# Performance work log

Hardware: AMD Instinct MI355X
Metric: run time of the kernel (lower is better)

Reference implementation:

```python
import jax, jax.numpy as jnp
import numpy as np

N, T, D = 2048, 32, 256
NE = T + 2                       # num_embeddings = 32 + 3 - 1
GK_MUL, GK_NUM = 2.0, 3
HEADS = (4, 1)

def _bn(x, g, b):
    # BatchNorm1d (training-mode batch stats, biased variance, eps=1e-5)
    m = x.mean(0)
    v = jnp.mean((x - m) ** 2, 0)
    return (x - m) * jax.lax.rsqrt(v + 1e-5) * g + b

def _gk(x):
    # multi-bandwidth Gaussian kernel over pairwise squared L2 distances
    sq = jnp.sum(x * x, -1)
    l2 = jnp.maximum(sq[:, None] + sq[None, :] - 2.0 * (x @ x.T), 0.0)
    n = x.shape[0]
    bw = jnp.sum(l2) / (n * n - n) / (GK_MUL ** (GK_NUM // 2))
    out = jnp.zeros_like(l2)
    for i in range(GK_NUM):
        out = out + jnp.exp(-l2 / (bw * (GK_MUL ** i)))
    return out

def _mlp3(x, w, b):
    h = jax.nn.relu(x @ w[0] + b[0])
    h = jax.nn.relu(h @ w[1] + b[1])
    return h @ w[2] + b[2]

def _ln(x, g, b):
    m = x.mean(-1, keepdims=True)
    v = jnp.mean((x - m) ** 2, -1, keepdims=True)
    return (x - m) * jax.lax.rsqrt(v + 1e-5) * g + b

def _posenc(t, d):
    pos = jnp.arange(t, dtype=jnp.float32)[:, None]
    div = jnp.exp(jnp.arange(0, d, 2, dtype=jnp.float32) * (-np.log(10000.0) / d))
    ang = pos * div
    return jnp.stack([jnp.sin(ang), jnp.cos(ang)], -1).reshape(t, d)

def _tlayer(x, mask, w, b, w1, b1, w2, b2, g, be, h):
    n, l, d = x.shape
    dh = d // h
    def split(t):
        return t.reshape(n, l, h, dh).transpose(0, 2, 1, 3)
    q = split(x @ w[0] + b[0])
    k = split(x @ w[1] + b[1])
    v = split(x @ w[2] + b[2])
    s = jnp.einsum('bhld,bhmd->bhlm', q, k) / np.sqrt(dh)
    s = jnp.where(mask[:, None, :, :], s, -1e9)
    o = jnp.einsum('bhlm,bhmd->bhld', jax.nn.softmax(s, -1), v)
    o = o.transpose(0, 2, 1, 3).reshape(n, l, d)
    x = _ln(x + o @ w[3] + b[3], g[0], be[0])
    f = jax.nn.relu(x @ w1 + b1) @ w2 + b2
    return _ln(x + f, g[1], be[1])

def _forward(emb0, emb1, emb2, simi_w, simi_b, bn_g, bn_b, simi_eps, dissim,
             gcn_w, gcn_b, adapt_w, adapt_b, type_emb, attn_w, attn_b,
             ffn_w1, ffn_b1, ffn_w2, ffn_b2, ln_g, ln_b,
             out_w1, out_b1, out_w2, out_b2, msk0, msk1, msk2):
    n = emb0.shape[0]
    embs = [emb0[:, 0, :], emb1, emb2]
    msks = [msk0[:, :1], msk1, msk2]               # [n,1] bool each
    mstk = jnp.stack(msks)                         # [3,n,1]
    mask_mats = mstk & jnp.swapaxes(mstk, 1, 2)    # [3,n,n]
    sim_sum = jnp.zeros((n, n), emb0.dtype)
    lstab = jnp.zeros((), emb0.dtype)
    for m in range(3):
        e = embs[m]
        p = _mlp3(e, simi_w[m], simi_b[m])
        wgk = _gk(_bn(jax.nn.relu(p), bn_g, bn_b))
        gk = _gk(_bn(e, bn_g, bn_b))
        eps = jax.nn.sigmoid(simi_eps[m])
        sim_sum = sim_sum + ((1.0 - eps) * wgk + eps) * gk * mask_mats[m]
        lstab = lstab + jnp.abs(jnp.linalg.norm(p) - jnp.linalg.norm(e))
    agg = sim_sum / mask_mats.sum(0).astype(emb0.dtype)
    agg = agg * (agg > jax.nn.sigmoid(dissim[0]))
    imputed = []
    for m in range(3):  # all modals are missing-capable
        h = jax.nn.relu(agg @ (embs[m] @ gcn_w[m, 0]) + gcn_b[m, 0])
        h = jax.nn.relu(agg @ (h @ gcn_w[m, 1]) + gcn_b[m, 1])
        s = jax.nn.sigmoid(embs[m] @ adapt_w[m].T + adapt_b[m])
        o = jax.nn.sigmoid(h @ adapt_w[m].T + adapt_b[m])  # adapt_self reused, bug kept from source
        s = s / (s + o)
        imp = s * embs[m] + (1.0 - s) * h
        mk = msks[m].astype(emb0.dtype)
        imputed.append(imp * mk + (1.0 - mk) * h)
    e0 = emb0.at[:, 0, :].set(imputed[0]) + type_emb[0]
    e0 = e0 + _posenc(emb0.shape[1], emb0.shape[2])
    e1 = imputed[1][:, None, :] + type_emb[1]
    e2 = imputed[2][:, None, :] + type_emb[2]
    z = jnp.concatenate([e0, e1, e2], 1)            # [n, NE, D]
    tok = jnp.concatenate([msk0, msk1, msk2], 1)    # [n, NE]
    amask = tok[:, :, None] & tok[:, None, :]       # [n, NE, NE]
    for li in range(2):
        z = jax.nn.relu(_tlayer(z, amask, attn_w[li], attn_b[li],
                                ffn_w1[li], ffn_b1[li], ffn_w2[li], ffn_b2[li],
                                ln_g[li], ln_b[li], HEADS[li]))
    comb = z.reshape(n, -1)
    y = jax.nn.relu(comb @ out_w1 + out_b1)
    y = (y @ out_w2 + out_b2).squeeze(-1)
    return y, lstab

def setup_inputs():
    key = jax.random.key(0)
    it = iter(jax.random.split(key, 32))
    def nrm(shape, s):
        return jax.random.normal(next(it), shape, jnp.float32) * s
    return {
        'emb0': nrm((N, T, D), 1.0),
        'emb1': nrm((N, D), 1.0),
        'emb2': nrm((N, D), 1.0),
        'msk0': jax.random.randint(next(it), (N, T), 0, 2).astype(bool),
        'msk1': jnp.ones((N, 1), bool),
        'msk2': jax.random.randint(next(it), (N, 1), 0, 2).astype(bool),
        'simi_w': nrm((3, 3, D, D), 0.06), 'simi_b': jnp.zeros((3, 3, D)),
        'bn_g': jnp.ones((D,)), 'bn_b': jnp.zeros((D,)),
        'simi_eps': jnp.ones((4,)), 'dissim': jnp.full((1,), 2.0),
        'gcn_w': nrm((3, 2, D, D), 0.06), 'gcn_b': jnp.zeros((3, 2, D)),
        'adapt_w': nrm((3, 1, D), 0.06), 'adapt_b': jnp.zeros((3, 1)),
        'type_emb': nrm((3, D), 0.02),
        'attn_w': nrm((2, 4, D, D), 0.06), 'attn_b': jnp.zeros((2, 4, D)),
        'ffn_w1': nrm((2, D, 4 * D), 0.06), 'ffn_b1': jnp.zeros((2, 4 * D)),
        'ffn_w2': nrm((2, 4 * D, D), 0.06), 'ffn_b2': jnp.zeros((2, D)),
        'ln_g': jnp.ones((2, 2, D)), 'ln_b': jnp.zeros((2, 2, D)),
        'out_w1': nrm((NE * D, 2 * D), 0.02), 'out_b1': jnp.zeros((2 * D,)),
        'out_w2': nrm((2 * D, 1), 0.02), 'out_b2': jnp.zeros((1,)),
    }

def reference(emb0, emb1, emb2, msk0, msk1, msk2, simi_w, simi_b, bn_g, bn_b,
              simi_eps, dissim, gcn_w, gcn_b, adapt_w, adapt_b, type_emb,
              attn_w, attn_b, ffn_w1, ffn_b1, ffn_w2, ffn_b2, ln_g, ln_b,
              out_w1, out_b1, out_w2, out_b2):
    return _forward(emb0, emb1, emb2, simi_w, simi_b, bn_g, bn_b, simi_eps,
                    dissim, gcn_w, gcn_b, adapt_w, adapt_b, type_emb, attn_w,
                    attn_b, ffn_w1, ffn_b1, ffn_w2, ffn_b2, ln_g, ln_b,
                    out_w1, out_b1, out_w2, out_b2, msk0, msk1, msk2)
```

## Files before the change

kernel.cpp:

```cpp
#include <hip/hip_runtime.h>
#include <hip/hip_bf16.h>


#define NN 2048
#define DD 256
#define LTOK 34

typedef __attribute__((ext_vector_type(8))) short bf16x8;
typedef __attribute__((ext_vector_type(4))) float f32x4;

__device__ __forceinline__ float bf2f(__hip_bfloat16 x) { return __bfloat162float(x); }
__device__ __forceinline__ __hip_bfloat16 f2bf(float x) { return __float2bfloat16(x); }
__device__ __forceinline__ float us2f(ushort u) {
    unsigned x = (unsigned)u << 16;
    float f;
    __builtin_memcpy(&f, &x, 4);
    return f;
}
__device__ __forceinline__ ushort f2us(float x) {
    __hip_bfloat16 h = f2bf(x);
    ushort u;
    __builtin_memcpy(&u, &h, 2);
    return u;
}

__device__ __forceinline__ float block_reduce_sum256(float v, float* red) {
    for (int o = 32; o > 0; o >>= 1) v += __shfl_down(v, o, 64);
    int tid = threadIdx.x;
    if ((tid & 63) == 0) red[tid >> 6] = v;
    __syncthreads();
    float s = red[0] + red[1] + red[2] + red[3];
    __syncthreads();
    return s;
}

__device__ __forceinline__ int xcd_remap(int lin, int nwg) {
    int q = nwg >> 3, r = nwg & 7;
    int xcd = lin & 7, pos = lin >> 3;
    return (xcd < r ? xcd * (q + 1) : r * (q + 1) + (xcd - r) * q) + pos;
}

__device__ __forceinline__ void stage_tile(const ushort* __restrict__ src,
                                           ushort* lds, int grow0, size_t ldk,
                                           int k0, int wv, int l) {
#pragma unroll
    for (int c = 0; c < 4; ++c) {
        int rowbase = wv * 32 + c * 8;
        int row = rowbase + (l >> 3);
        int sx = ((l & 7) ^ (row & 7)) * 8;
        __builtin_amdgcn_global_load_lds(
            (const __attribute__((address_space(1))) void*)(src + (size_t)(grow0 + row) * ldk + k0 + sx),
            (__attribute__((address_space(3))) void*)(lds + rowbase * 64), 16, 0, 0);
    }
}

__device__ __forceinline__ void stage_tile64(const ushort* __restrict__ src,
                                             ushort* lds, int grow0, size_t ldk,
                                             int k0, int wv, int l) {
#pragma unroll
    for (int c = 0; c < 2; ++c) {
        int rowbase = wv * 16 + c * 8;
        int row = rowbase + (l >> 3);
        int sx = ((l & 7) ^ (row & 7)) * 8;
        __builtin_amdgcn_global_load_lds(
            (const __attribute__((address_space(1))) void*)(src + (size_t)(grow0 + row) * ldk + k0 + sx),
            (__attribute__((address_space(3))) void*)(lds + rowbase * 64), 16, 0, 0);
    }
}

#define MFMA_STEP(ACC)                                                          \
    {                                                                           \
        bf16x8 av[4], bv[4];                                                    \
        _Pragma("unroll") for (int f = 0; f < 4; ++f) {                         \
            int ra = wr * 64 + f * 16 + lr;                                     \
            av[f] = *(const bf16x8*)(As + ra * 64 + (((kk * 4 + l16) ^ (ra & 7)) * 8)); \
            int rb = wc * 64 + f * 16 + lr;                                     \
            bv[f] = *(const bf16x8*)(Bs + rb * 64 + (((kk * 4 + l16) ^ (rb & 7)) * 8)); \
        }                                                                       \
        _Pragma("unroll") for (int mf = 0; mf < 4; ++mf)                        \
            _Pragma("unroll") for (int nf = 0; nf < 4; ++nf)                    \
                ACC[mf][nf] = __builtin_amdgcn_mfma_f32_16x16x32_bf16(          \
                    av[mf], bv[nf], ACC[mf][nf], 0, 0, 0);                      \
    }

#define MFMA_STEP_T(ACC)                                                        \
    {                                                                           \
        bf16x8 av[2], bv[4];                                                    \
        _Pragma("unroll") for (int f = 0; f < 2; ++f) {                         \
            int ra = wr * 32 + f * 16 + lr;                                     \
            av[f] = *(const bf16x8*)(As + ra * 64 + (((kk * 4 + l16) ^ (ra & 7)) * 8)); \
        }                                                                       \
        _Pragma("unroll") for (int f = 0; f < 4; ++f) {                         \
            int rb = wc * 64 + f * 16 + lr;                                     \
            bv[f] = *(const bf16x8*)(Bs + rb * 64 + (((kk * 4 + l16) ^ (rb & 7)) * 8)); \
        }                                                                       \
        _Pragma("unroll") for (int mf = 0; mf < 2; ++mf)                        \
            _Pragma("unroll") for (int nf = 0; nf < 4; ++nf)                    \
                ACC[mf][nf] = __builtin_amdgcn_mfma_f32_16x16x32_bf16(          \
                    av[mf], bv[nf], ACC[mf][nf], 0, 0, 0);                      \
    }

template <int OUTM, bool BIAS, bool RELU>
__global__ __launch_bounds__(256) void gemm_mfma(
    const ushort* __restrict__ A, const ushort* __restrict__ Bt,
    const float* __restrict__ bias, void* __restrict__ Cout,
    int M, int N, int K)
{
    __shared__ __align__(16) ushort As[128 * 64];
    __shared__ __align__(16) ushort Bs[128 * 64];
    const int gx = gridDim.x;
    int lin = xcd_remap(blockIdx.y * gx + blockIdx.x, gx * gridDim.y);
    const int bm = (lin / gx) * 128, bn = (lin % gx) * 128;
    const int tid = threadIdx.x;
    const int l = tid & 63, wv = tid >> 6;
    const int wr = wv >> 1, wc = wv & 1;
    const int l16 = l >> 4, lr = l & 15;
    const int kpz = K / gridDim.z;
    const int kbeg = blockIdx.z * kpz, kend = kbeg + kpz;
    f32x4 zero = {0.f, 0.f, 0.f, 0.f};
    f32x4 acc[4][4];
#pragma unroll
    for (int i = 0; i < 4; ++i)
#pragma unroll
        for (int j = 0; j < 4; ++j) acc[i][j] = zero;

    for (int k0 = kbeg; k0 < kend; k0 += 64) {
        stage_tile(A, As, bm, K, k0, wv, l);
        stage_tile(Bt, Bs, bn, K, k0, wv, l);
        __syncthreads();
#pragma unroll
        for (int kk = 0; kk < 2; ++kk) MFMA_STEP(acc)
        __syncthreads();
    }
    float* Cf = (float*)Cout + (size_t)blockIdx.z * M * N;
    __hip_bfloat16* Cb = (__hip_bfloat16*)Cout + (size_t)blockIdx.z * M * N;
#pragma unroll
    for (int mf = 0; mf < 4; ++mf) {
#pragma unroll
        for (int nf = 0; nf < 4; ++nf) {
            int col = bn + wc * 64 + nf * 16 + lr;
            float bb = BIAS ? bias[col] : 0.f;
#pragma unroll
            for (int r = 0; r < 4; ++r) {
                int row = bm + wr * 64 + mf * 16 + l16 * 4 + r;
                float v = acc[mf][nf][r] + bb;
                if (OUTM == 3)
                    v += bf2f(((const __hip_bfloat16*)Cout)[(size_t)row * N + col]);
                if (RELU) v = fmaxf(v, 0.f);
                if (OUTM == 0)
                    Cf[(size_t)row * N + col] = v;
                else if (OUTM == 5)
                    Cb[(size_t)row * N + col] = f2bf(v);
                else
                    ((__hip_bfloat16*)Cout)[(size_t)row * N + col] = f2bf(v);
            }
        }
    }
}

template <int OUTM, bool BIAS, bool RELU>
__global__ __launch_bounds__(256) void gemm_thin(
    const ushort* __restrict__ A, const ushort* __restrict__ Bt,
    const float* __restrict__ bias, void* __restrict__ Cout,
    int M, int N, int K)
{
    __shared__ __align__(16) ushort As[64 * 64];
    __shared__ __align__(16) ushort Bs[128 * 64];
    const int gx = gridDim.x;
    int lin = xcd_remap(blockIdx.y * gx + blockIdx.x, gx * gridDim.y);
    const int bm = (lin / gx) * 64, bn = (lin % gx) * 128;
    const int tid = threadIdx.x;
    const int l = tid & 63, wv = tid >> 6;
    const int wr = wv >> 1, wc = wv & 1;
    const int l16 = l >> 4, lr = l & 15;
    f32x4 zero = {0.f, 0.f, 0.f, 0.f};
    f32x4 acc[2][4];
#pragma unroll
    for (int i = 0; i < 2; ++i)
#pragma unroll
        for (int j = 0; j < 4; ++j) acc[i][j] = zero;

    for (int k0 = 0; k0 < K; k0 += 64) {
        stage_tile64(A, As, bm, K, k0, wv, l);
        stage_tile(Bt, Bs, bn, K, k0, wv, l);
        __syncthreads();
#pragma unroll
        for (int kk = 0; kk < 2; ++kk) MFMA_STEP_T(acc)
        __syncthreads();
    }
#pragma unroll
    for (int mf = 0; mf < 2; ++mf) {
#pragma unroll
        for (int nf = 0; nf < 4; ++nf) {
            int col = bn + wc * 64 + nf * 16 + lr;
            float bb = BIAS ? bias[col] : 0.f;
#pragma unroll
            for (int r = 0; r < 4; ++r) {
                int row = bm + wr * 32 + mf * 16 + l16 * 4 + r;
                float v = acc[mf][nf][r] + bb;
                if (OUTM == 3)
                    v += bf2f(((const __hip_bfloat16*)Cout)[(size_t)row * N + col]);
                if (RELU) v = fmaxf(v, 0.f);
                ((__hip_bfloat16*)Cout)[(size_t)row * N + col] = f2bf(v);
            }
        }
    }
}

template <int OUTM, bool RELU, bool BIAS, bool PSUM>
__global__ __launch_bounds__(256) void gemm_batch_t(
    const ushort* __restrict__ A, int lda, size_t aoffZ,
    const ushort* __restrict__ Bt, size_t boffZ,
    const float* __restrict__ bias, int biasoffZ,
    void* __restrict__ Cout, int ldc, size_t coffZ,
    float* __restrict__ psum, int M, int N, int K)
{
    __shared__ __align__(16) ushort As[64 * 64];
    __shared__ __align__(16) ushort Bs[128 * 64];
    __shared__ float red[8];
    const int gx = gridDim.x;
    const int lin0 = blockIdx.y * gx + blockIdx.x;
    int lin = xcd_remap(lin0, gx * gridDim.y);
    const int bm = (lin / gx) * 64, bn = (lin % gx) * 128;
    const int z = blockIdx.z;
    A += (size_t)z * aoffZ;
    Bt += (size_t)z * boffZ;
    if (BIAS) bias += (size_t)z * biasoffZ;
    const int tid = threadIdx.x;
    const int l = tid & 63, wv = tid >> 6;
    const int wr = wv >> 1, wc = wv & 1;
    const int l16 = l >> 4, lr = l & 15;
    f32x4 zero = {0.f, 0.f, 0.f, 0.f};
    f32x4 acc[2][4];
#pragma unroll
    for (int i = 0; i < 2; ++i)
#pragma unroll
        for (int j = 0; j < 4; ++j) acc[i][j] = zero;

    for (int k0 = 0; k0 < K; k0 += 64) {
        stage_tile64(A, As, bm, lda, k0, wv, l);
        stage_tile(Bt, Bs, bn, K, k0, wv, l);
        __syncthreads();
#pragma unroll
        for (int kk = 0; kk < 2; ++kk) MFMA_STEP_T(acc)
        __syncthreads();
    }
    float lsq = 0.f;
#pragma unroll
    for (int mf = 0; mf < 2; ++mf) {
#pragma unroll
        for (int nf = 0; nf < 4; ++nf) {
            int col = bn + wc * 64 + nf * 16 + lr;
            float bb = BIAS ? bias[col] : 0.f;
#pragma unroll
            for (int r = 0; r < 4; ++r) {
                int row = bm + wr * 32 + mf * 16 + l16 * 4 + r;
                float v = acc[mf][nf][r] + bb;
                if (RELU) v = fmaxf(v, 0.f);
                if (PSUM) lsq += v * v;
                if (OUTM == 0)
                    ((float*)Cout + (size_t)z * coffZ)[(size_t)row * ldc + col] = v;
                else if (OUTM == 2)
                    ((__hip_bfloat16*)Cout + (size_t)z * coffZ)[(size_t)col * M + row] = f2bf(v);
                else
                    ((__hip_bfloat16*)Cout + (size_t)z * coffZ)[(size_t)row * ldc + col] = f2bf(v);
            }
        }
    }
    if (PSUM) {
        float bs = block_reduce_sum256(lsq, red);
        if (tid == 0) psum[z * gx * gridDim.y + lin0] = bs;
    }
}

__global__ __launch_bounds__(256) void gemm_dist_gk3(
    const ushort* __restrict__ XB6, const float* __restrict__ SQ6,
    const float* __restrict__ bws, const int* __restrict__ MK,
    const float* __restrict__ epsp, ushort* __restrict__ S3b)
{
    __shared__ __align__(16) ushort As[64 * 64];
    __shared__ __align__(16) ushort Bs[128 * 64];
    const int gx = gridDim.x;
    int lin = xcd_remap(blockIdx.y * gx + blockIdx.x, gx * gridDim.y);
    const int bm = (lin / gx) * 64, bn = (lin % gx) * 128;
    const int z = blockIdx.z;
    const ushort* XB = XB6 + (size_t)(2 * z) * NN * DD;
    const float* SQ = SQ6 + (size_t)(2 * z) * NN;
    const int* mk = MK + (size_t)z * NN;
    ushort* S = S3b + (size_t)z * NN * NN;
    const int tid = threadIdx.x;
    const int l = tid & 63, wv = tid >> 6;
    const int wr = wv >> 1, wc = wv & 1;
    const int l16 = l >> 4, lr = l & 15;
    f32x4 zero = {0.f, 0.f, 0.f, 0.f};
    f32x4 acc1[2][4], acc2[2][4];
#pragma unroll
    for (int i = 0; i < 2; ++i)
#pragma unroll
        for (int j = 0; j < 4; ++j) { acc1[i][j] = zero; acc2[i][j] = zero; }

    for (int k0 = 0; k0 < 256; k0 += 64) {
        stage_tile64(XB, As, bm, 256, k0, wv, l);
        stage_tile(XB, Bs, bn, 256, k0, wv, l);
        __syncthreads();
#pragma unroll
        for (int kk = 0; kk < 2; ++kk) MFMA_STEP_T(acc1)
        __syncthreads();
    }
    const ushort* X1 = XB + (size_t)NN * DD;
    for (int k0 = 0; k0 < 256; k0 += 64) {
        stage_tile64(X1, As, bm, 256, k0, wv, l);
        stage_tile(X1, Bs, bn, 256, k0, wv, l);
        __syncthreads();
#pragma unroll
        for (int kk = 0; kk < 2; ++kk) MFMA_STEP_T(acc2)
        __syncthreads();
    }
    float eps = 1.f / (1.f + __expf(-epsp[z]));
    const float cnn = 1.f / ((float)NN * NN - (float)NN);
    float ia4 = 0.5f / (bws[2 * z] * cnn);
    float ib4 = 0.5f / (bws[2 * z + 1] * cnn);
#pragma unroll
    for (int mf = 0; mf < 2; ++mf) {
#pragma unroll
        for (int nf = 0; nf < 4; ++nf) {
            int col = bn + wc * 64 + nf * 16 + lr;
            int mcol = mk[col];
            float sqc0 = SQ[col], sqc1 = SQ[NN + col];
#pragma unroll
            for (int r = 0; r < 4; ++r) {
                int row = bm + wr * 32 + mf * 16 + l16 * 4 + r;
                float d1 = fmaxf(SQ[row] + sqc0 - 2.f * acc1[mf][nf][r], 0.f);
                float d2 = fmaxf(SQ[NN + row] + sqc1 - 2.f * acc2[mf][nf][r], 0.f);
                float t = __expf(-d1 * ia4);
                float t2 = t * t;
                float w = t + t2 + t2 * t2;
                float u = __expf(-d2 * ib4);
                float u2 = u * u;
                float g = u + u2 + u2 * u2;
                float val = ((1.f - eps) * w + eps) * g;
                val = (mk[row] && mcol) ? val : 0.f;
                S[(size_t)row * NN + col] = f2us(val);
            }
        }
    }
}

__global__ __launch_bounds__(256) void bw_fast6(const float* __restrict__ SQ6,
                                                const float* __restrict__ bnb,
                                                float* __restrict__ SCbw) {
    __shared__ float red[8];
    int z = blockIdx.x, tid = threadIdx.x;
    float s1p = 0.f;
    for (int r = tid; r < NN; r += 256) s1p += SQ6[z * NN + r];
    float b = bnb[tid];
    float s1 = block_reduce_sum256(s1p, red);
    float b2 = block_reduce_sum256(b * b, red);
    if (tid == 0)
        SCbw[z] = 2.f * (float)NN * s1 - 2.f * (float)NN * (float)NN * b2;
}

template <int Z, bool RELU>
__global__ __launch_bounds__(256) void slice_fin_b(const ushort4* __restrict__ SL,
                                                   const float* __restrict__ bias,
                                                   __hip_bfloat16* __restrict__ out,
                                                   int N, size_t MN) {
    size_t v = (size_t)blockIdx.x * 256 + threadIdx.x;
    size_t MN4 = MN >> 2;
    float sx = 0.f, sy = 0.f, sz = 0.f, sw = 0.f;
#pragma unroll
    for (int z = 0; z < Z; ++z) {
        ushort4 t = SL[(size_t)z * MN4 + v];
        sx += us2f(t.x); sy += us2f(t.y); sz += us2f(t.z); sw += us2f(t.w);
    }
    float4 bb = ((const float4*)bias)[v % (size_t)(N >> 2)];
    sx += bb.x; sy += bb.y; sz += bb.z; sw += bb.w;
    if (RELU) {
        sx = fmaxf(sx, 0.f); sy = fmaxf(sy, 0.f);
        sz = fmaxf(sz, 0.f); sw = fmaxf(sw, 0.f);
    }
    union { __hip_bfloat16 h[4]; ushort4 u; } pk;
    pk.h[0] = f2bf(sx); pk.h[1] = f2bf(sy);
    pk.h[2] = f2bf(sz); pk.h[3] = f2bf(sw);
    ((ushort4*)out)[v] = pk.u;
}

__global__ void cvt_flat(const float* __restrict__ in, __hip_bfloat16* __restrict__ out,
                         int n4) {
    int i = blockIdx.x * 256 + threadIdx.x;
    if (i < n4) {
        float4 v = ((const float4*)in)[i];
        union { __hip_bfloat16 h[4]; ushort4 u; } pk;
        pk.h[0] = f2bf(v.x); pk.h[1] = f2bf(v.y);
        pk.h[2] = f2bf(v.z); pk.h[3] = f2bf(v.w);
        ((ushort4*)out)[i] = pk.u;
    }
}

__global__ __launch_bounds__(256) void cvt_transz(const float* __restrict__ in,
                                                  __hip_bfloat16* __restrict__ out,
                                                  int R, int C) {
    __shared__ float t[32][33];
    size_t zo = (size_t)blockIdx.z * R * C;
    in += zo;
    out += zo;
    int bc = blockIdx.x * 32, br = blockIdx.y * 32;
    int tx = threadIdx.x & 31, ty = threadIdx.x >> 5;
#pragma unroll
    for (int i = 0; i < 32; i += 8)
        t[ty + i][tx] = in[(size_t)(br + ty + i) * C + bc + tx];
    __syncthreads();
#pragma unroll
    for (int i = 0; i < 32; i += 8)
        out[(size_t)(bc + ty + i) * R + br + tx] = f2bf(t[tx][ty + i]);
}

__global__ __launch_bounds__(256) void agg_cvt3(
    const ushort4* __restrict__ S3b, const int* __restrict__ mk0,
    const int* __restrict__ mk1, const int* __restrict__ mk2,
    const float* __restrict__ dissim, ushort4* __restrict__ Sb) {
    size_t v = (size_t)blockIdx.x * 256 + threadIdx.x;
    const size_t PL = (size_t)NN * NN / 4;
    int i = (int)(v >> 9);
    int j0 = (int)((v & 511) << 2);
    float thr = 1.f / (1.f + __expf(-dissim[0]));
    ushort4 u0 = S3b[v], u1 = S3b[PL + v], u2 = S3b[2 * PL + v];
    int m0i = mk0[i], m1i = mk1[i], m2i = mk2[i];
    union { __hip_bfloat16 h[4]; ushort4 u; } pk;
#define AGGC(C0, C1, C2, J)                                                       \
    {                                                                             \
        int j = j0 + J;                                                           \
        int cnt = ((m0i && mk0[j]) ? 1 : 0) + ((m1i && mk1[j]) ? 1 : 0) +         \
                  ((m2i && mk2[j]) ? 1 : 0);                                      \
        float a = cnt ? (us2f(C0) + us2f(C1) + us2f(C2)) / (float)cnt : 0.f;      \
        pk.h[J] = f2bf((a > thr) ? a : 0.f);                                      \
    }
    AGGC(u0.x, u1.x, u2.x, 0) AGGC(u0.y, u1.y, u2.y, 1)
    AGGC(u0.z, u1.z, u2.z, 2) AGGC(u0.w, u1.w, u2.w, 3)
#undef AGGC
    Sb[v] = pk.u;
}

__global__ __launch_bounds__(256) void colstats6(const float* __restrict__ P3,
                                                 const float* __restrict__ E0,
                                                 const float* __restrict__ e1,
                                                 const float* __restrict__ e2,
                                                 float* __restrict__ mv, int nrows) {
    __shared__ float red[8];
    int c = blockIdx.x, z = blockIdx.y, tid = threadIdx.x;
    int m = z >> 1, kind = z & 1;
    const float* X = kind ? (m == 0 ? E0 : (m == 1 ? e1 : e2))
                          : P3 + (size_t)m * NN * DD;
    float s = 0.f, sq = 0.f;
    for (int r = tid; r < nrows; r += 256) {
        float v = X[(size_t)r * DD + c];
        if (!kind) v = fmaxf(v, 0.f);
        s += v; sq += v * v;
    }
    float ts = block_reduce_sum256(s, red);
    float tq = block_reduce_sum256(sq, red);
    if (tid == 0) {
        float mmean = ts / (float)nrows;
        mv[z * 512 + c] = mmean;
        mv[z * 512 + 256 + c] = tq / (float)nrows - mmean * mmean;
    }
}

__global__ __launch_bounds__(256) void bn_fuse6(const float* __restrict__ P3,
                                                const float* __restrict__ E0,
                                                const float* __restrict__ e1,
                                                const float* __restrict__ e2,
                                                const float* __restrict__ mv,
                                                const float* __restrict__ g,
                                                const float* __restrict__ b,
                                                ushort* __restrict__ XB6,
                                                float* __restrict__ SQ6) {
    __shared__ float red[8];
    int r = blockIdx.x, z = blockIdx.y, c = threadIdx.x;
    int m = z >> 1, kind = z & 1;
    const float* X = kind ? (m == 0 ? E0 : (m == 1 ? e1 : e2))
                          : P3 + (size_t)m * NN * DD;
    float v = X[(size_t)r * DD + c];
    if (!kind) v = fmaxf(v, 0.f);
    float y = (v - mv[z * 512 + c]) * rsqrtf(mv[z * 512 + 256 + c] + 1e-5f) * g[c] + b[c];
    __hip_bfloat16 yb = f2bf(y);
    XB6[(size_t)z * NN * DD + (size_t)r * DD + c] = *(ushort*)&yb;
    float yr = bf2f(yb);
    float s = block_reduce_sum256(yr * yr, red);
    if (c == 0) SQ6[z * NN + r] = s;
}

__global__ __launch_bounds__(256) void sumsq3(const float* __restrict__ X0,
                                              const float* __restrict__ X1,
                                              const float* __restrict__ X2,
                                              int n, float* __restrict__ part) {
    __shared__ float red[8];
    int z = blockIdx.y, tid = threadIdx.x;
    const float* X = (z == 0) ? X0 : ((z == 1) ? X1 : X2);
    float s = 0.f;
    for (size_t idx = (size_t)blockIdx.x * 256 + tid; idx < (size_t)n;
         idx += (size_t)gridDim.x * 256) {
        float v = X[idx];
        s += v * v;
    }
    float bs = block_reduce_sum256(s, red);
    if (tid == 0) part[512 + z * 512 + blockIdx.x] = bs;
}

__global__ __launch_bounds__(256) void reduce6(const float* __restrict__ part,
                                               float* __restrict__ SC) {
    __shared__ float red[8];
    int b = blockIdx.x, tid = threadIdx.x;
    const float* src; int n, dst;
    if (b < 3) { src = part + 512 + b * 512; n = 512; dst = 9 + b; }
    else { src = part + 2048 + (b - 3) * 64; n = 64; dst = 6 + (b - 3); }
    float s = 0.f;
    for (int i = tid; i < n; i += 256) s += src[i];
    float bs = block_reduce_sum256(s, red);
    if (tid == 0) SC[dst] = bs;
}

__global__ __launch_bounds__(256) void impute_k(
    const float* __restrict__ E, const __hip_bfloat16* __restrict__ H, int ldh,
    const float* __restrict__ aw, const float* __restrict__ ab,
    const int* __restrict__ mk, float* __restrict__ OUT) {
    __shared__ float red[8];
    int i = blockIdx.x, tid = threadIdx.x;
    float e = E[(size_t)i * DD + tid], h = bf2f(H[(size_t)i * ldh + tid]), w = aw[tid];
    float se = block_reduce_sum256(e * w, red);
    float sh = block_reduce_sum256(h * w, red);
    float s = 1.f / (1.f + __expf(-(se + ab[0])));
    float o = 1.f / (1.f + __expf(-(sh + ab[0])));
    s = s / (s + o);
    float imp = s * e + (1.f - s) * h;
    float m = mk[i] ? 1.f : 0.f;
    OUT[(size_t)i * DD + tid] = imp * m + (1.f - m) * h;
}

__global__ void detect_mode(const void* __restrict__ m1, int* __restrict__ modep) {
    if (threadIdx.x == 0 && blockIdx.x == 0) {
        int vi = ((const int*)m1)[0];
        float vf = ((const float*)m1)[0];
        modep[0] = (vi == 1) ? 0 : ((vf == 1.0f) ? 2 : 1);
    }
}

__device__ __forceinline__ int rd_mask(const void* p, int idx, int mode) {
    if (mode == 0) return ((const int*)p)[idx] != 0;
    if (mode == 1) return ((const unsigned char*)p)[idx] != 0;
    return ((const float*)p)[idx] != 0.f;
}

__global__ void build_masks(const void* __restrict__ m0, const void* __restrict__ m1,
                            const void* __restrict__ m2, const int* __restrict__ modep,
                            int* __restrict__ MK, int* __restrict__ TOK) {
    int mode = modep[0];
    int idx = blockIdx.x * 256 + threadIdx.x;
    if (idx < NN) {
        MK[idx] = rd_mask(m0, idx * 32, mode);
        MK[NN + idx] = rd_mask(m1, idx, mode);
        MK[2 * NN + idx] = rd_mask(m2, idx, mode);
    }
    if (idx < NN * LTOK) {
        int i = idx / LTOK, t = idx - i * LTOK;
        TOK[idx] = (t < 32) ? rd_mask(m0, i * 32 + t, mode)
                            : ((t == 32) ? rd_mask(m1, i, mode) : rd_mask(m2, i, mode));
    }
}

__global__ void gather_e0(const float* __restrict__ emb0, float* __restrict__ E0,
                          __hip_bfloat16* __restrict__ E0b) {
    int i = blockIdx.x, c = threadIdx.x;
    float v = emb0[(size_t)i * 32 * DD + c];
    E0[(size_t)i * DD + c] = v;
    E0b[(size_t)i * DD + c] = f2bf(v);
}

__global__ void pe_table(const float* __restrict__ type_emb, float* __restrict__ PET) {
    int t = blockIdx.x, c = threadIdx.x;
    float div = __expf((float)((c >> 1) << 1) * (-9.210340371976184f / 256.f));
    float ang = (float)t * div;
    float pe = (c & 1) ? __cosf(ang) : __sinf(ang);
    PET[t * 256 + c] = type_emb[c] + pe;
}

__global__ void build_z2(const float4* __restrict__ emb0, const float4* __restrict__ i0,
                         const float4* __restrict__ i1, const float4* __restrict__ i2,
                         const float4* __restrict__ PET,
                         const float4* __restrict__ type_emb,
                         ushort4* __restrict__ Z) {
    int idx = blockIdx.x * 256 + threadIdx.x;
    int c4 = idx & 63;
    int t = (idx >> 6) % LTOK;
    int i = idx / (LTOK * 64);
    float4 v, a;
    if (t < 32) {
        v = (t == 0) ? i0[(size_t)i * 64 + c4]
                     : emb0[((size_t)i * 32 + t) * 64 + c4];
        a = PET[t * 64 + c4];
    } else if (t == 32) {
        v = i1[(size_t)i * 64 + c4];
        a = type_emb[64 + c4];
    } else {
        v = i2[(size_t)i * 64 + c4];
        a = type_emb[128 + c4];
    }
    union { __hip_bfloat16 h[4]; ushort4 u; } pk;
    pk.h[0] = f2bf(v.x + a.x); pk.h[1] = f2bf(v.y + a.y);
    pk.h[2] = f2bf(v.z + a.z); pk.h[3] = f2bf(v.w + a.w);
    Z[idx] = pk.u;
}

template <int DH, int NH>
__global__ __launch_bounds__(256) void attn_mfma(
    const ushort* __restrict__ QKV, const int* __restrict__ tok,
    __hip_bfloat16* __restrict__ O, int sample0)
{
    __shared__ float S_lds[48][49];
    __shared__ ushort P_lds[48][72];
    __shared__ __align__(16) ushort VT_lds[256 * 42 + 64];
    __shared__ int tok_lds[34];
    const int s = blockIdx.x;
    const int tid = threadIdx.x;
    const int wv = tid >> 6, l = tid & 63, lr = l & 15, l16 = l >> 4;
    const int rowQ = s * 34;
    if (tid < 34) tok_lds[tid] = tok[(size_t)(sample0 + s) * LTOK + tid];
    for (int idx = tid; idx < 256 * 8 + 64; idx += 256) {
        int d = idx >> 3, jp = 34 + (idx & 7);
        int off = (idx < 2048) ? d * 42 + jp : 256 * 42 + (idx - 2048);
        VT_lds[off] = 0;
    }
    for (int idx = tid; idx < 34 * 256; idx += 256) {
        int j = idx >> 8, d = idx & 255;
        VT_lds[d * 42 + j] = QKV[(size_t)(rowQ + j) * 768 + 512 + d];
    }
    const float scale = rsqrtf((float)DH);
    __syncthreads();
#pragma unroll
    for (int h = 0; h < NH; ++h) {
        for (int t = wv; t < 9; t += 4) {
            int mj = t / 3, ni = t % 3;
            f32x4 acc = {0.f, 0.f, 0.f, 0.f};
#pragma unroll
            for (int ks = 0; ks < DH / 32; ++ks) {
                bf16x8 a = *(const bf16x8*)(QKV +
                    (size_t)(rowQ + mj * 16 + lr) * 768 + 256 + h * DH + ks * 32 + l16 * 8);
                bf16x8 b = *(const bf16x8*)(QKV +
                    (size_t)(rowQ + ni * 16 + lr) * 768 + h * DH + ks * 32 + l16 * 8);
                acc = __builtin_amdgcn_mfma_f32_16x16x32_bf16(a, b, acc, 0, 0, 0);
            }
#pragma unroll
            for (int r = 0; r < 4; ++r)
                S_lds[mj * 16 + l16 * 4 + r][ni * 16 + lr] = acc[r];
        }
        __syncthreads();
        if (tid < 48) {
            int i = tid;
            if (i < 34) {
                int ti = tok_lds[i];
                float sc[34];
                float mx = -1e30f;
#pragma unroll
                for (int j = 0; j < 34; ++j) {
                    float v = (ti && tok_lds[j]) ? S_lds[j][i] * scale : -1e9f;
                    sc[j] = v;
                    mx = fmaxf(mx, v);
                }
                float sum = 0.f;
#pragma unroll
                for (int j = 0; j < 34; ++j) {
                    sc[j] = __expf(sc[j] - mx);
                    sum += sc[j];
                }
                float inv = 1.f / sum;
#pragma unroll
                for (int j = 0; j < 34; ++j) P_lds[i][j] = f2us(sc[j] * inv);
#pragma unroll
                for (int j = 34; j < 64; ++j) P_lds[i][j] = 0;
            } else {
#pragma unroll
                for (int j = 0; j < 64; ++j) P_lds[i][j] = 0;
            }
        }
        __syncthreads();
        for (int nt = wv; nt < DH / 16; nt += 4) {
            f32x4 acc[3];
#pragma unroll
            for (int mi = 0; mi < 3; ++mi) acc[mi] = (f32x4){0.f, 0.f, 0.f, 0.f};
#pragma unroll
            for (int ks = 0; ks < 2; ++ks) {
                int j0 = ks * 32 + l16 * 8;
                int d = h * DH + nt * 16 + lr;
                bf16x8 bv;
                __builtin_memcpy(&bv, VT_lds + d * 42 + j0, 16);
#pragma unroll
                for (int mi = 0; mi < 3; ++mi) {
                    bf16x8 av = *(const bf16x8*)(&P_lds[0][0] + (mi * 16 + lr) * 72 + j0);
                    acc[mi] = __builtin_amdgcn_mfma_f32_16x16x32_bf16(av, bv, acc[mi], 0, 0, 0);
                }
            }
#pragma unroll
            for (int mi = 0; mi < 3; ++mi)
#pragma unroll
                for (int r = 0; r < 4; ++r) {
                    int i = mi * 16 + l16 * 4 + r;
                    if (i < 34)
                        O[(size_t)(rowQ + i) * 256 + h * DH + nt * 16 + lr] =
                            f2bf(acc[mi][r]);
                }
        }
        __syncthreads();
    }
}

template <bool RELU>
__global__ __launch_bounds__(256) void ln_rows(__hip_bfloat16* __restrict__ Z,
                                               const float* __restrict__ g,
                                               const float* __restrict__ b) {
    int row = (blockIdx.x << 2) + (threadIdx.x >> 6);
    int l = threadIdx.x & 63;
    ushort4 u = ((ushort4*)(Z + (size_t)row * DD))[l];
    float x0 = us2f(u.x), x1 = us2f(u.y), x2 = us2f(u.z), x3 = us2f(u.w);
    float s = x0 + x1 + x2 + x3;
    for (int o = 1; o < 64; o <<= 1) s += __shfl_xor(s, o, 64);
    float mean = s * (1.f / 256.f);
    float d0 = x0 - mean, d1 = x1 - mean, d2 = x2 - mean, d3 = x3 - mean;
    float q = d0 * d0 + d1 * d1 + d2 * d2 + d3 * d3;
    for (int o = 1; o < 64; o <<= 1) q += __shfl_xor(q, o, 64);
    float rst = rsqrtf(q * (1.f / 256.f) + 1e-5f);
    float4 gg = ((const float4*)g)[l], bb = ((const float4*)b)[l];
    float y0 = d0 * rst * gg.x + bb.x, y1 = d1 * rst * gg.y + bb.y;
    float y2 = d2 * rst * gg.z + bb.z, y3 = d3 * rst * gg.w + bb.w;
    if (RELU) {
        y0 = fmaxf(y0, 0.f); y1 = fmaxf(y1, 0.f);
        y2 = fmaxf(y2, 0.f); y3 = fmaxf(y3, 0.f);
    }
    union { __hip_bfloat16 h[4]; ushort4 v; } pk;
    pk.h[0] = f2bf(y0); pk.h[1] = f2bf(y1); pk.h[2] = f2bf(y2); pk.h[3] = f2bf(y3);
    ((ushort4*)(Z + (size_t)row * DD))[l] = pk.v;
}

__global__ __launch_bounds__(256) void head2(const __hip_bfloat16* __restrict__ Y1,
                                             const float* __restrict__ w,
                                             const float* __restrict__ b,
                                             float* __restrict__ out) {
    __shared__ float red[8];
    int i = blockIdx.x, tid = threadIdx.x;
    float s = bf2f(Y1[(size_t)i * 512 + tid]) * w[tid] +
              bf2f(Y1[(size_t)i * 512 + 256 + tid]) * w[256 + tid];
    float bs = block_reduce_sum256(s, red);
    if (tid == 0) out[i] = bs + b[0];
}

__global__ void lstab_k(const float* __restrict__ SC, float* __restrict__ dst) {
    if (threadIdx.x == 0 && blockIdx.x == 0) {
        float s = 0.f;
        for (int m = 0; m < 3; ++m)
            s += fabsf(sqrtf(SC[6 + m]) - sqrtf(SC[9 + m]));
        dst[0] = s;
    }
}

__global__ void gcn_bias_cat(const float* __restrict__ gcn_b, float* __restrict__ Bcat) {
    int m = blockIdx.x, l = blockIdx.y, c = threadIdx.x;
    Bcat[l * 768 + m * 256 + c] = gcn_b[(m * 2 + l) * 256 + c];
}

#define GEMM(OUTM_, BIAS_, RELU_, A_, Bt_, BI_, C_, M_, N_, K_)                 \
    gemm_mfma<OUTM_, BIAS_, RELU_>                                              \
        <<<dim3((N_) / 128, (M_) / 128), 256, 0, stream>>>(                     \
            (const ushort*)(A_), (const ushort*)(Bt_), (BI_), (void*)(C_),      \
            (M_), (N_), (K_))
#define GEMMZ(A_, Bt_, C_, M_, N_, K_, Z_)                                      \
    gemm_mfma<5, false, false>                                                  \
        <<<dim3((N_) / 128, (M_) / 128, (Z_)), 256, 0, stream>>>(               \
            (const ushort*)(A_), (const ushort*)(Bt_), (const float*)nullptr,   \
            (void*)(C_), (M_), (N_), (K_))
#define GEMMT(OUTM_, BIAS_, RELU_, A_, Bt_, BI_, C_, M_, N_, K_)                \
    gemm_thin<OUTM_, BIAS_, RELU_>                                              \
        <<<dim3((N_) / 128, (M_) / 64), 256, 0, stream>>>(                      \
            (const ushort*)(A_), (const ushort*)(Bt_), (BI_), (void*)(C_),      \
            (M_), (N_), (K_))

extern "C" void kernel_launch(void* const* d_in, const int* in_sizes, int n_in,
                              void* d_out, int out_size, void* d_ws, size_t ws_size,
                              hipStream_t stream) {
    (void)in_sizes; (void)n_in; (void)out_size; (void)ws_size;
    const float* emb0 = (const float*)d_in[0];
    const float* emb1 = (const float*)d_in[1];
    const float* emb2 = (const float*)d_in[2];
    const void* msk0 = d_in[3];
    const void* msk1 = d_in[4];
    const void* msk2 = d_in[5];
    const float* simi_w = (const float*)d_in[6];
    const float* simi_b = (const float*)d_in[7];
    const float* bn_g = (const float*)d_in[8];
    const float* bn_b = (const float*)d_in[9];
    const float* simi_eps = (const float*)d_in[10];
    const float* dissim = (const float*)d_in[11];
    const float* gcn_w = (const float*)d_in[12];
    const float* gcn_b = (const float*)d_in[13];
    const float* adapt_w = (const float*)d_in[14];
    const float* adapt_b = (const float*)d_in[15];
    const float* type_emb = (const float*)d_in[16];
    const float* attn_w = (const float*)d_in[17];
    const float* attn_b = (const float*)d_in[18];
    const float* ffn_w1 = (const float*)d_in[19];
    const float* ffn_b1 = (const float*)d_in[20];
    const float* ffn_w2 = (const float*)d_in[21];
    const float* ffn_b2 = (const float*)d_in[22];
    const float* ln_g = (const float*)d_in[23];
    const float* ln_b = (const float*)d_in[24];
    const float* out_w1 = (const float*)d_in[25];
    const float* out_b1 = (const float*)d_in[26];
    const float* out_w2 = (const float*)d_in[27];
    const float* out_b2 = (const float*)d_in[28];
    float* out = (float*)d_out;

    const int ACH = 1024, ACROWS = ACH * LTOK;

    char* wp = (char*)d_ws;
    auto alloc = [&](size_t bytes) -> char* {
        char* p = wp;
        wp += (bytes + 255) & ~(size_t)255;
        return p;
    };
    __hip_bfloat16* Zb = (__hip_bfloat16*)alloc((size_t)NN * LTOK * DD * 2);
    char* UN = alloc((size_t)80 * 1024 * 1024);
    ushort* S3b = (ushort*)UN;
    __hip_bfloat16* QKVb = (__hip_bfloat16*)UN;
    __hip_bfloat16* Ob = (__hip_bfloat16*)(UN + (size_t)ACROWS * 768 * 2);
    __hip_bfloat16* Hfb = (__hip_bfloat16*)UN;
    __hip_bfloat16* SLICEB = (__hip_bfloat16*)UN;
    __hip_bfloat16* Sb = (__hip_bfloat16*)alloc((size_t)NN * NN * 2);
    float* P3 = (float*)alloc((size_t)3 * NN * DD * 4);
    float* E0 = (float*)alloc((size_t)NN * DD * 4);
    __hip_bfloat16* Eb3 = (__hip_bfloat16*)alloc((size_t)3 * NN * DD * 2);
    __hip_bfloat16* T1b3 = (__hip_bfloat16*)alloc((size_t)3 * NN * DD * 2);
    __hip_bfloat16* T2b3 = (__hip_bfloat16*)alloc((size_t)3 * NN * DD * 2);
    ushort* XB6 = (ushort*)alloc((size_t)6 * NN * DD * 2);
    __hip_bfloat16* TBt3 = (__hip_bfloat16*)alloc((size_t)3 * NN * DD * 2);
    __hip_bfloat16* HB3 = (__hip_bfloat16*)alloc((size_t)NN * 768 * 2);
    __hip_bfloat16* HB2_3 = (__hip_bfloat16*)alloc((size_t)NN * 768 * 2);
    float* I0 = (float*)alloc((size_t)NN * DD * 4);
    float* I1 = (float*)alloc((size_t)NN * DD * 4);
    float* I2 = (float*)alloc((size_t)NN * DD * 4);
    __hip_bfloat16* Y1b = (__hip_bfloat16*)alloc((size_t)NN * 512 * 2);
    __hip_bfloat16* simi_wt = (__hip_bfloat16*)alloc((size_t)9 * 65536 * 2);
    __hip_bfloat16* gcn_wt = (__hip_bfloat16*)alloc((size_t)6 * 65536 * 2);
    __hip_bfloat16* attn_wt = (__hip_bfloat16*)alloc((size_t)8 * 65536 * 2);
    __hip_bfloat16* w1t = (__hip_bfloat16*)alloc((size_t)2 * 262144 * 2);
    __hip_bfloat16* w2t = (__hip_bfloat16*)alloc((size_t)2 * 262144 * 2);
    __hip_bfloat16* ow1t = (__hip_bfloat16*)alloc((size_t)8704 * 512 * 2);
    float* PET = (float*)alloc(32 * 256 * 4);
    float* MV6 = (float*)alloc(6 * 512 * 4);
    float* SQ6 = (float*)alloc(6 * NN * 4);
    float* PART = (float*)alloc(4096 * 4);
    float* SC = (float*)alloc(64 * 4);
    float* Bcat = (float*)alloc(1536 * 4);
    int* TOK = (int*)alloc((size_t)NN * LTOK * 4);
    int* MK = (int*)alloc((size_t)3 * NN * 4);

    cvt_transz<<<dim3(8, 8, 9), 256, 0, stream>>>(simi_w, simi_wt, 256, 256);
    cvt_transz<<<dim3(8, 8, 6), 256, 0, stream>>>(gcn_w, gcn_wt, 256, 256);
    cvt_transz<<<dim3(8, 8, 8), 256, 0, stream>>>(attn_w, attn_wt, 256, 256);
    cvt_transz<<<dim3(32, 8, 2), 256, 0, stream>>>(ffn_w1, w1t, 256, 1024);
    cvt_transz<<<dim3(8, 32, 2), 256, 0, stream>>>(ffn_w2, w2t, 1024, 256);
    cvt_transz<<<dim3(16, 272, 1), 256, 0, stream>>>(out_w1, ow1t, 8704, 512);

    pe_table<<<32, 256, 0, stream>>>(type_emb, PET);
    gather_e0<<<NN, 256, 0, stream>>>(emb0, E0, Eb3);
    cvt_flat<<<512, 256, 0, stream>>>(emb1, Eb3 + (size_t)NN * DD, NN * DD / 4);
    cvt_flat<<<512, 256, 0, stream>>>(emb2, Eb3 + (size_t)2 * NN * DD, NN * DD / 4);
    detect_mode<<<1, 64, 0, stream>>>(msk1, (int*)SC + 16);
    build_masks<<<(NN * LTOK + 255) / 256, 256, 0, stream>>>(msk0, msk1, msk2,
                                                             (int*)SC + 16, MK, TOK);
    gcn_bias_cat<<<dim3(3, 2), 256, 0, stream>>>(gcn_b, Bcat);

    const float* Ef[3] = {E0, emb1, emb2};

    sumsq3<<<dim3(512, 3), 256, 0, stream>>>(E0, emb1, emb2, NN * DD, PART);
    gemm_batch_t<1, true, true, false><<<dim3(2, 32, 3), 256, 0, stream>>>(
        (const ushort*)Eb3, 256, (size_t)NN * DD, (const ushort*)simi_wt,
        (size_t)3 * 65536, simi_b, 3 * 256, T1b3, 256, (size_t)NN * DD,
        nullptr, NN, 256, 256);
    gemm_batch_t<1, true, true, false><<<dim3(2, 32, 3), 256, 0, stream>>>(
        (const ushort*)T1b3, 256, (size_t)NN * DD, (const ushort*)(simi_wt + 65536),
        (size_t)3 * 65536, simi_b + 256, 3 * 256, T2b3, 256, (size_t)NN * DD,
        nullptr, NN, 256, 256);
    gemm_batch_t<0, false, true, true><<<dim3(2, 32, 3), 256, 0, stream>>>(
        (const ushort*)T2b3, 256, (size_t)NN * DD, (const ushort*)(simi_wt + 2 * 65536),
        (size_t)3 * 65536, simi_b + 2 * 256, 3 * 256, P3, 256, (size_t)NN * DD,
        PART + 2048, NN, 256, 256);
    reduce6<<<6, 256, 0, stream>>>(PART, SC);

    colstats6<<<dim3(256, 6), 256, 0, stream>>>(P3, E0, emb1, emb2, MV6, NN);
    bn_fuse6<<<dim3(NN, 6), 256, 0, stream>>>(P3, E0, emb1, emb2, MV6, bn_g, bn_b,
                                              XB6, SQ6);
    bw_fast6<<<6, 256, 0, stream>>>(SQ6, bn_b, SC + 20);

    gemm_dist_gk3<<<dim3(16, 32, 3), 256, 0, stream>>>(XB6, SQ6, SC + 20, MK,
                                                       simi_eps, S3b);

    agg_cvt3<<<4096, 256, 0, stream>>>((const ushort4*)S3b, MK, MK + NN, MK + 2 * NN,
                                       dissim, (ushort4*)Sb);
    gemm_batch_t<2, false, false, false><<<dim3(2, 32, 3), 256, 0, stream>>>(
        (const ushort*)Eb3, 256, (size_t)NN * DD, (const ushort*)gcn_wt,
        (size_t)2 * 65536, nullptr, 0, TBt3, 256, (size_t)NN * DD,
        nullptr, NN, 256, 256);
    GEMMZ(Sb, TBt3, SLICEB, NN, 768, NN, 8);
    slice_fin_b<8, true><<<1536, 256, 0, stream>>>((const ushort4*)SLICEB, Bcat, HB3,
                                                   768, (size_t)NN * 768);
    gemm_batch_t<2, false, false, false><<<dim3(2, 32, 3), 256, 0, stream>>>(
        (const ushort*)HB3, 768, (size_t)256, (const ushort*)(gcn_wt + 65536),
        (size_t)2 * 65536, nullptr, 0, TBt3, 256, (size_t)NN * DD,
        nullptr, NN, 256, 256);
    GEMMZ(Sb, TBt3, SLICEB, NN, 768, NN, 8);
    slice_fin_b<8, true><<<1536, 256, 0, stream>>>((const ushort4*)SLICEB, Bcat + 768,
                                                   HB2_3, 768, (size_t)NN * 768);
    float* IMP[3] = {I0, I1, I2};
    for (int m = 0; m < 3; ++m)
        impute_k<<<NN, 256, 0, stream>>>(Ef[m], HB2_3 + m * 256, 768,
                                         adapt_w + m * 256, adapt_b + m,
                                         MK + m * NN, IMP[m]);

    build_z2<<<NN * LTOK * 64 / 256, 256, 0, stream>>>(
        (const float4*)emb0, (const float4*)I0, (const float4*)I1, (const float4*)I2,
        (const float4*)PET, (const float4*)type_emb, (ushort4*)Zb);
    const int NCHUNK = NN / ACH;
    for (int li = 0; li < 2; ++li) {
        for (int c = 0; c < NCHUNK; ++c) {
            __hip_bfloat16* Zc = Zb + (size_t)c * ACROWS * DD;
            GEMMT(1, true, false, Zc, attn_wt + (size_t)(li * 4) * 65536,
                  attn_b + li * 4 * 256, QKVb, ACROWS, 768, 256);
            if (li == 0)
                attn_mfma<64, 4><<<ACH, 256, 0, stream>>>(
                    (const ushort*)QKVb, TOK, Ob, c * ACH);
            else
                attn_mfma<256, 1><<<ACH, 256, 0, stream>>>(
                    (const ushort*)QKVb, TOK, Ob, c * ACH);
            GEMMT(3, true, false, Ob, attn_wt + (size_t)(li * 4 + 3) * 65536,
                  attn_b + (li * 4 + 3) * 256, Zc, ACROWS, 256, 256);
        }
        ln_rows<false><<<NN * LTOK / 4, 256, 0, stream>>>(Zb, ln_g + (li * 2 + 0) * 256,
                                                          ln_b + (li * 2 + 0) * 256);
        for (int c = 0; c < NCHUNK; ++c) {
            __hip_bfloat16* Zc = Zb + (size_t)c * ACROWS * DD;
            GEMM(1, true, true, Zc, w1t + (size_t)li * 262144, ffn_b1 + li * 1024,
                 Hfb, ACROWS, 1024, 256);
            GEMMT(3, true, false, Hfb, w2t + (size_t)li * 262144, ffn_b2 + li * 256,
                  Zc, ACROWS, 256, 1024);
        }
        ln_rows<true><<<NN * LTOK / 4, 256, 0, stream>>>(Zb, ln_g + (li * 2 + 1) * 256,
                                                         ln_b + (li * 2 + 1) * 256);
    }

    GEMMZ(Zb, ow1t, SLICEB, NN, 512, LTOK * DD, 8);
    slice_fin_b<8, true><<<1024, 256, 0, stream>>>((const ushort4*)SLICEB, out_b1, Y1b,
                                                   512, (size_t)NN * 512);
    head2<<<NN, 256, 0, stream>>>(Y1b, out_w2, out_b2, out);
    lstab_k<<<1, 64, 0, stream>>>(SC, out + NN);
}
```

Measured before the change: 852.4 us.

## Fuse residual GEMM epilogue with LayerNorm in transformer layers

```diff
diff --git a/kernel.cpp b/kernel.cpp
--- a/kernel.cpp
+++ b/kernel.cpp
@@ -205,6 +205,107 @@
             }
         }
     }
+}
+
+template <bool RELU>
+__global__ __launch_bounds__(256) void gemm_thin_ln(
+    const ushort* __restrict__ A, const ushort* __restrict__ Bt,
+    const float* __restrict__ bias, __hip_bfloat16* __restrict__ C,
+    const float* __restrict__ g, const float* __restrict__ be,
+    int M, int K)
+{
+    __shared__ __align__(16) ushort As[64 * 64];
+    __shared__ __align__(16) ushort Bs[256 * 64];
+    __shared__ float rs[64][2], rq[64][2];
+    int lin = xcd_remap(blockIdx.y, gridDim.y);
+    const int bm = lin * 64;
+    const int tid = threadIdx.x;
+    const int l = tid & 63, wv = tid >> 6;
+    const int wr = wv >> 1, wc = wv & 1;
+    const int l16 = l >> 4, lr = l & 15;
+    f32x4 zero = {0.f, 0.f, 0.f, 0.f};
+    f32x4 acc[2][8];
+#pragma unroll
+    for (int i = 0; i < 2; ++i)
+#pragma unroll
+        for (int j = 0; j < 8; ++j) acc[i][j] = zero;
+
+    for (int k0 = 0; k0 < K; k0 += 64) {
+        stage_tile64(A, As, bm, K, k0, wv, l);
+        stage_tile(Bt, Bs, 0, K, k0, wv, l);
+        stage_tile(Bt, Bs + 128 * 64, 128, K, k0, wv, l);
+        __syncthreads();
+#pragma unroll
+        for (int kk = 0; kk < 2; ++kk) {
+            bf16x8 av[2];
+#pragma unroll
+            for (int f = 0; f < 2; ++f) {
+                int ra = wr * 32 + f * 16 + lr;
+                av[f] = *(const bf16x8*)(As + ra * 64 + (((kk * 4 + l16) ^ (ra & 7)) * 8));
+            }
+#pragma unroll
+            for (int nf = 0; nf < 8; ++nf) {
+                int rb = wc * 128 + nf * 16 + lr;
+                bf16x8 bv = *(const bf16x8*)(Bs + rb * 64 + (((kk * 4 + l16) ^ (rb & 7)) * 8));
+#pragma unroll
+                for (int mf = 0; mf < 2; ++mf)
+                    acc[mf][nf] = __builtin_amdgcn_mfma_f32_16x16x32_bf16(
+                        av[mf], bv, acc[mf][nf], 0, 0, 0);
+            }
+        }
+        __syncthreads();
+    }
+#pragma unroll
+    for (int mf = 0; mf < 2; ++mf)
+#pragma unroll
+        for (int nf = 0; nf < 8; ++nf) {
+            int col = wc * 128 + nf * 16 + lr;
+            float bb = bias[col];
+#pragma unroll
+            for (int r = 0; r < 4; ++r) {
+                int row = bm + wr * 32 + mf * 16 + l16 * 4 + r;
+                acc[mf][nf][r] += bb + bf2f(C[(size_t)row * 256 + col]);
+            }
+        }
+#pragma unroll
+    for (int mf = 0; mf < 2; ++mf)
+#pragma unroll
+        for (int r = 0; r < 4; ++r) {
+            float s = 0.f, q = 0.f;
+#pragma unroll
+            for (int nf = 0; nf < 8; ++nf) {
+                float v = acc[mf][nf][r];
+                s += v;
+                q += v * v;
+            }
+            for (int off = 1; off <= 8; off <<= 1) {
+                s += __shfl_xor(s, off, 64);
+                q += __shfl_xor(q, off, 64);
+            }
+            if (lr == 0) {
+                int rl = wr * 32 + mf * 16 + l16 * 4 + r;
+                rs[rl][wc] = s;
+                rq[rl][wc] = q;
+            }
+        }
+    __syncthreads();
+#pragma unroll
+    for (int mf = 0; mf < 2; ++mf)
+#pragma unroll
+        for (int r = 0; r < 4; ++r) {
+            int rl = wr * 32 + mf * 16 + l16 * 4 + r;
+            float mean = (rs[rl][0] + rs[rl][1]) * (1.f / 256.f);
+            float var = (rq[rl][0] + rq[rl][1]) * (1.f / 256.f) - mean * mean;
+            float rstd = rsqrtf(var + 1e-5f);
+            int row = bm + rl;
+#pragma unroll
+            for (int nf = 0; nf < 8; ++nf) {
+                int col = wc * 128 + nf * 16 + lr;
+                float y = (acc[mf][nf][r] - mean) * rstd * g[col] + be[col];
+                if (RELU) y = fmaxf(y, 0.f);
+                C[(size_t)row * 256 + col] = f2bf(y);
+            }
+        }
 }
 
 template <int OUTM, bool RELU, bool BIAS, bool PSUM>
@@ -711,33 +812,6 @@
         }
         __syncthreads();
     }
-}
-
-template <bool RELU>
-__global__ __launch_bounds__(256) void ln_rows(__hip_bfloat16* __restrict__ Z,
-                                               const float* __restrict__ g,
-                                               const float* __restrict__ b) {
-    int row = (blockIdx.x << 2) + (threadIdx.x >> 6);
-    int l = threadIdx.x & 63;
-    ushort4 u = ((ushort4*)(Z + (size_t)row * DD))[l];
-    float x0 = us2f(u.x), x1 = us2f(u.y), x2 = us2f(u.z), x3 = us2f(u.w);
-    float s = x0 + x1 + x2 + x3;
-    for (int o = 1; o < 64; o <<= 1) s += __shfl_xor(s, o, 64);
-    float mean = s * (1.f / 256.f);
-    float d0 = x0 - mean, d1 = x1 - mean, d2 = x2 - mean, d3 = x3 - mean;
-    float q = d0 * d0 + d1 * d1 + d2 * d2 + d3 * d3;
-    for (int o = 1; o < 64; o <<= 1) q += __shfl_xor(q, o, 64);
-    float rst = rsqrtf(q * (1.f / 256.f) + 1e-5f);
-    float4 gg = ((const float4*)g)[l], bb = ((const float4*)b)[l];
-    float y0 = d0 * rst * gg.x + bb.x, y1 = d1 * rst * gg.y + bb.y;
-    float y2 = d2 * rst * gg.z + bb.z, y3 = d3 * rst * gg.w + bb.w;
-    if (RELU) {
-        y0 = fmaxf(y0, 0.f); y1 = fmaxf(y1, 0.f);
-        y2 = fmaxf(y2, 0.f); y3 = fmaxf(y3, 0.f);
-    }
-    union { __hip_bfloat16 h[4]; ushort4 v; } pk;
-    pk.h[0] = f2bf(y0); pk.h[1] = f2bf(y1); pk.h[2] = f2bf(y2); pk.h[3] = f2bf(y3);
-    ((ushort4*)(Z + (size_t)row * DD))[l] = pk.v;
 }
 
 __global__ __launch_bounds__(256) void head2(const __hip_bfloat16* __restrict__ Y1,
@@ -939,20 +1013,22 @@
             else
                 attn_mfma<256, 1><<<ACH, 256, 0, stream>>>(
                     (const ushort*)QKVb, TOK, Ob, c * ACH);
-            GEMMT(3, true, false, Ob, attn_wt + (size_t)(li * 4 + 3) * 65536,
-                  attn_b + (li * 4 + 3) * 256, Zc, ACROWS, 256, 256);
-        }
-        ln_rows<false><<<NN * LTOK / 4, 256, 0, stream>>>(Zb, ln_g + (li * 2 + 0) * 256,
-                                                          ln_b + (li * 2 + 0) * 256);
+            gemm_thin_ln<false><<<dim3(1, ACROWS / 64), 256, 0, stream>>>(
+                (const ushort*)Ob, (const ushort*)(attn_wt + (size_t)(li * 4 + 3) * 65536),
+                attn_b + (li * 4 + 3) * 256, Zc,
+                ln_g + (li * 2 + 0) * 256, ln_b + (li * 2 + 0) * 256,
+                ACROWS, 256);
+        }
         for (int c = 0; c < NCHUNK; ++c) {
             __hip_bfloat16* Zc = Zb + (size_t)c * ACROWS * DD;
             GEMM(1, true, true, Zc, w1t + (size_t)li * 262144, ffn_b1 + li * 1024,
                  Hfb, ACROWS, 1024, 256);
-            GEMMT(3, true, false, Hfb, w2t + (size_t)li * 262144, ffn_b2 + li * 256,
-                  Zc, ACROWS, 256, 1024);
-        }
-        ln_rows<true><<<NN * LTOK / 4, 256, 0, stream>>>(Zb, ln_g + (li * 2 + 1) * 256,
-                                                         ln_b + (li * 2 + 1) * 256);
+            gemm_thin_ln<true><<<dim3(1, ACROWS / 64), 256, 0, stream>>>(
+                (const ushort*)Hfb, (const ushort*)(w2t + (size_t)li * 262144),
+                ffn_b2 + li * 256, Zc,
+                ln_g + (li * 2 + 1) * 256, ln_b + (li * 2 + 1) * 256,
+                ACROWS, 1024);
+        }
     }
 
     GEMMZ(Zb, ow1t, SLICEB, NN, 512, LTOK * DD, 8);
```

New measurement: 907.8 us. 1.06x slower.
